# Optimization experiments

Measured on AMD Instinct MI355X. Metric: run time of the kernel, lower is better.

Reference implementation:

```python
import jax, jax.numpy as jnp
from jax import lax
import numpy as np

V, E, H, T, L = 100000, 300, 512, 11, 4096
START, STOP = 9, 10
NEG_INF = -10000.0


def setup_inputs() -> dict:
    key = jax.random.key(0)
    ks = jax.random.split(key, 14)
    n = lambda k, s, sc=0.1: jax.random.normal(k, s, dtype=jnp.float32) * sc
    transitions = jax.random.normal(ks[12], (T, T), dtype=jnp.float32)
    # __init__ pins transitions into START and out of STOP
    transitions = transitions.at[START, :].set(NEG_INF).at[:, STOP].set(NEG_INF)
    return {
        'sentence': jax.random.randint(ks[0], (L,), 0, V),
        'embedding': n(ks[1], (V, E), 1.0),
        'w_ih_f': n(ks[2], (4 * H, E)), 'w_hh_f': n(ks[3], (4 * H, H)),
        'b_ih_f': n(ks[4], (4 * H,)), 'b_hh_f': n(ks[5], (4 * H,)),
        'w_ih_b': n(ks[6], (4 * H, E)), 'w_hh_b': n(ks[7], (4 * H, H)),
        'b_ih_b': n(ks[8], (4 * H,)), 'b_hh_b': n(ks[9], (4 * H,)),
        'w_tag': n(ks[10], (T, 2 * H)), 'b_tag': n(ks[11], (T,)),
        'transitions': transitions,
    }


def _lstm(x, w_ih, w_hh, b_ih, b_hh, reverse):
    # x: [L, E]; PyTorch gate order i, f, g, o
    Hd = w_hh.shape[1]
    # precompute input projections for all timesteps: [L, 4H]
    xg = x @ w_ih.T + b_ih + b_hh
    def step(carry, xt):
        h, c = carry
        g = xt + w_hh @ h
        i, f, gg, o = jnp.split(g, 4)
        c = jax.nn.sigmoid(f) * c + jax.nn.sigmoid(i) * jnp.tanh(gg)
        h = jax.nn.sigmoid(o) * jnp.tanh(c)
        return (h, c), h
    init = (jnp.zeros((Hd,), x.dtype), jnp.zeros((Hd,), x.dtype))
    _, hs = lax.scan(step, init, xg, reverse=reverse)
    return hs  # [L, H]


def _get_lstm_features(sentence, embedding, w_ih_f, w_hh_f, b_ih_f, b_hh_f,
                       w_ih_b, w_hh_b, b_ih_b, b_hh_b, w_tag, b_tag):
    x = embedding[sentence]  # [L, E]
    hf = _lstm(x, w_ih_f, w_hh_f, b_ih_f, b_hh_f, reverse=False)
    hb = _lstm(x, w_ih_b, w_hh_b, b_ih_b, b_hh_b, reverse=True)
    h = jnp.concatenate([hf, hb], axis=-1)  # [L, 2H]
    return h @ w_tag.T + b_tag  # [L, T]


def _viterbi(feats, transitions):
    init = jnp.full((T,), NEG_INF, feats.dtype).at[START].set(0.0)
    def step(fv, feat):
        scores = fv[None, :] + transitions  # [T_next, T_prev]
        bptr = jnp.argmax(scores, axis=1)
        fv2 = jnp.max(scores, axis=1) + feat
        return fv2, bptr
    fv, bptrs = lax.scan(step, init, feats)  # bptrs: [L, T]
    terminal = fv + transitions[STOP]
    best = jnp.argmax(terminal)
    path_score = terminal[best]
    def back(tag, bp):
        return bp[tag], tag
    _, path = lax.scan(back, best, bptrs, reverse=True)  # tags for t=0..L-1
    return path_score, path


def reference(sentence, embedding, w_ih_f, w_hh_f, b_ih_f, b_hh_f,
              w_ih_b, w_hh_b, b_ih_b, b_hh_b, w_tag, b_tag, transitions):
    feats = _get_lstm_features(sentence, embedding, w_ih_f, w_hh_f, b_ih_f, b_hh_f,
                               w_ih_b, w_hh_b, b_ih_b, b_hh_b, w_tag, b_tag)
    return _viterbi(feats, transitions)
```

## Files before the change

kernel.cpp:

```cpp
#include <hip/hip_runtime.h>
#include <hip/hip_bf16.h>
#include <stdint.h>

#define LL 4096
#define EE 300
#define HH 512
#define G4H 2048
#define TT 11
#define TSTART 9
#define TSTOP 10
#define NEGINF -10000.0f

typedef unsigned long long u64;
typedef short short8 __attribute__((ext_vector_type(8)));
typedef float f32x4 __attribute__((ext_vector_type(4)));

__device__ __forceinline__ float sigf(float x){
    x = fminf(fmaxf(x, -30.f), 30.f);
    return 1.0f / (1.0f + __expf(-x));
}
__device__ __forceinline__ float tanhfast(float x){
    x = fminf(fmaxf(x, -15.f), 15.f);
    float e = __expf(-2.0f * x);
    return (1.0f - e) / (1.0f + e);
}
__device__ __forceinline__ u64 lda(const u64* p){
    return __hip_atomic_load(p, __ATOMIC_RELAXED, __HIP_MEMORY_SCOPE_AGENT);
}
__device__ __forceinline__ unsigned f2bf(float f){
    unsigned u = __float_as_uint(f);
    return ((u + 0x7FFFu + ((u >> 16) & 1u)) >> 16) & 0xFFFFu;
}

__global__ void k0_zero(u64* __restrict__ comm){
    int i = blockIdx.x * blockDim.x + threadIdx.x;
    if (i < 2 * 2 * HH) comm[i] = 0ull;
}

__global__ __launch_bounds__(256) void k1_xg(
    const int* __restrict__ sent, const float* __restrict__ emb,
    const float* __restrict__ wih_f, const float* __restrict__ bih_f, const float* __restrict__ bhh_f,
    const float* __restrict__ wih_b, const float* __restrict__ bih_b, const float* __restrict__ bhh_b,
    float* __restrict__ xg_f, float* __restrict__ xg_b)
{
    __shared__ float elds[32 * 304];
    int t0  = blockIdx.x * 32;
    int r0  = blockIdx.y * 256;
    int dir = blockIdx.z;
    const float* wih = dir ? wih_b : wih_f;
    const float* bih = dir ? bih_b : bih_f;
    const float* bhh = dir ? bhh_b : bhh_f;
    float* xg = dir ? xg_b : xg_f;

    for (int idx = threadIdx.x; idx < 32 * EE; idx += 256){
        int i = idx / EE, e = idx - i * EE;
        elds[i * 304 + e] = emb[(long)sent[t0 + i] * EE + e];
    }
    __syncthreads();

    int rA = r0 + (threadIdx.x & 127);
    int rB = rA + 128;
    int half = threadIdx.x >> 7;
    float accA[16], accB[16];
    #pragma unroll
    for (int i = 0; i < 16; i++){ accA[i] = 0.f; accB[i] = 0.f; }
    const float* wrowA = wih + (long)rA * EE;
    const float* wrowB = wih + (long)rB * EE;
    for (int e4 = 0; e4 < 75; e4++){
        float4 wa = *reinterpret_cast<const float4*>(wrowA + e4 * 4);
        float4 wb = *reinterpret_cast<const float4*>(wrowB + e4 * 4);
        #pragma unroll
        for (int i = 0; i < 16; i++){
            float4 ev = *reinterpret_cast<const float4*>(&elds[(half * 16 + i) * 304 + e4 * 4]);
            accA[i] += wa.x * ev.x + wa.y * ev.y + wa.z * ev.z + wa.w * ev.w;
            accB[i] += wb.x * ev.x + wb.y * ev.y + wb.z * ev.z + wb.w * ev.w;
        }
    }
    float bA = bih[rA] + bhh[rA];
    float bB = bih[rB] + bhh[rB];
    #pragma unroll
    for (int i = 0; i < 16; i++){
        int t = t0 + half * 16 + i;
        xg[(long)t * G4H + rA] = accA[i] + bA;
        xg[(long)t * G4H + rB] = accB[i] + bB;
    }
}

__global__ __launch_bounds__(256) void k2_lstm(
    const float* __restrict__ whh_f, const float* __restrict__ whh_b,
    const float* __restrict__ xg_f, const float* __restrict__ xg_b,
    float* __restrict__ hs_f, float* __restrict__ hs_b,
    u64* __restrict__ comm)
{
    int dir = blockIdx.x >> 5;
    int b   = blockIdx.x & 31;
    int j0  = b * 16;
    int tid = threadIdx.x;
    int v   = tid >> 6;
    int l   = tid & 63;
    int grp = l >> 4;
    int jmine = j0 + v * 4 + grp;

    const float* whh = dir ? whh_b : whh_f;
    const float* xg  = dir ? xg_b  : xg_f;
    float* hs        = dir ? hs_b  : hs_f;
    u64* cm          = comm + dir * 2 * HH;

    short8 afrag[16];
    {
        int m    = l & 15;
        int jloc = m >> 2;
        int g    = m & 3;
        const float* wp = whh + (size_t)(g * HH + j0 + v * 4 + jloc) * HH + (l >> 4) * 8;
        #pragma unroll
        for (int kc = 0; kc < 16; kc++){
            float4 w0 = *reinterpret_cast<const float4*>(wp + kc * 32);
            float4 w1 = *reinterpret_cast<const float4*>(wp + kc * 32 + 4);
            union { unsigned u[4]; short8 s; } fr;
            fr.u[0] = f2bf(w0.x) | (f2bf(w0.y) << 16);
            fr.u[1] = f2bf(w0.z) | (f2bf(w0.w) << 16);
            fr.u[2] = f2bf(w1.x) | (f2bf(w1.y) << 16);
            fr.u[3] = f2bf(w1.z) | (f2bf(w1.w) << 16);
            afrag[kc] = fr.s;
        }
    }

    __shared__ __align__(16) unsigned hb[2][256];
    float c = 0.f;

    for (int s = 0; s < LL; ++s){
        int t = dir ? (LL - 1 - s) : s;

        const float* xp = xg + (size_t)t * G4H + jmine;
        float xg0 = xp[0], xg1 = xp[HH], xg2 = xp[2 * HH], xg3 = xp[3 * HH];

        if (s > 0){
            u64* pw = cm + (s & 1) * HH + 2 * tid;
            u64 va = lda(pw), vb = lda(pw + 1);
            unsigned want = (unsigned)s;
            for (;;){
                bool ok = ((unsigned)(va >> 32) == want) && ((unsigned)(vb >> 32) == want);
                if (__all(ok)) break;
                if ((unsigned)(va >> 32) != want) va = lda(pw);
                if ((unsigned)(vb >> 32) != want) vb = lda(pw + 1);
            }
            hb[s & 1][tid] = f2bf(__uint_as_float((unsigned)va))
                           | (f2bf(__uint_as_float((unsigned)vb)) << 16);
        }
        __syncthreads();

        f32x4 acc = {0.f, 0.f, 0.f, 0.f};
        if (s > 0){
            const char* hbase = (const char*)&hb[s & 1][0] + grp * 16;
            #pragma unroll
            for (int kc = 0; kc < 16; kc++){
                short8 bfrag = *reinterpret_cast<const short8*>(hbase + kc * 64);
                acc = __builtin_amdgcn_mfma_f32_16x16x32_bf16(afrag[kc], bfrag, acc, 0, 0, 0);
            }
        }

        float vi = acc[0] + xg0;
        float vf = acc[1] + xg1;
        float vgg = acc[2] + xg2;
        float vo = acc[3] + xg3;
        c = sigf(vf) * c + sigf(vi) * tanhfast(vgg);
        float hv = sigf(vo) * tanhfast(c);

        if ((l & 15) == 0){
            union { float f; unsigned u; } cv; cv.f = hv;
            u64 pk = ((u64)(s + 1) << 32) | (u64)cv.u;
            __hip_atomic_store(cm + ((s + 1) & 1) * HH + jmine, pk,
                               __ATOMIC_RELAXED, __HIP_MEMORY_SCOPE_AGENT);
            hs[(size_t)t * HH + jmine] = hv;
        }
    }
}

__global__ __launch_bounds__(64) void k3_feats(
    const float* __restrict__ hs_f, const float* __restrict__ hs_b,
    const float* __restrict__ wtag, const float* __restrict__ btag,
    float* __restrict__ feats)
{
    int t = blockIdx.x;
    int lane = threadIdx.x;
    float hreg[16];
    #pragma unroll
    for (int q = 0; q < 16; q++){
        int k = q * 64 + lane;
        hreg[q] = (q < 8) ? hs_f[(long)t * HH + k] : hs_b[(long)t * HH + (k - HH)];
    }
    for (int n = 0; n < TT; n++){
        float a = 0.f;
        #pragma unroll
        for (int q = 0; q < 16; q++){
            a += wtag[n * 1024 + q * 64 + lane] * hreg[q];
        }
        #pragma unroll
        for (int off = 32; off; off >>= 1) a += __shfl_down(a, off, 64);
        if (lane == 0) feats[t * 12 + n] = a + btag[n];
    }
}

__global__ __launch_bounds__(64) void k4a_chunk(
    const float* __restrict__ feats, const float* __restrict__ trans,
    float* __restrict__ Pmat)
{
    int c = blockIdx.x;
    int lane = threadIdx.x;
    float tr[TT][TT];
    #pragma unroll
    for (int n = 0; n < TT; n++)
        #pragma unroll
        for (int p = 0; p < TT; p++) tr[n][p] = trans[n * TT + p];

    float pv[TT];
    #pragma unroll
    for (int n = 0; n < TT; n++) pv[n] = (n == lane) ? 0.f : NEGINF;

    for (int i = 0; i < 64; i++){
        int t = c * 64 + i;
        float ft[TT];
        #pragma unroll
        for (int n = 0; n < TT; n++) ft[n] = feats[t * 12 + n];
        float pn[TT];
        #pragma unroll
        for (int n = 0; n < TT; n++){
            float m = tr[n][0] + pv[0];
            #pragma unroll
            for (int p = 1; p < TT; p++) m = fmaxf(m, tr[n][p] + pv[p]);
            pn[n] = m + ft[n];
        }
        #pragma unroll
        for (int n = 0; n < TT; n++) pv[n] = pn[n];
    }
    if (lane < TT){
        #pragma unroll
        for (int n = 0; n < TT; n++) Pmat[(c * TT + n) * TT + lane] = pv[n];
    }
}

__global__ __launch_bounds__(64) void k4b_bound(
    const float* __restrict__ Pmat, float* __restrict__ fvb)
{
    int lane = threadIdx.x;
    int ln = (lane < TT) ? lane : 0;
    float fv[TT];
    #pragma unroll
    for (int n = 0; n < TT; n++) fv[n] = (n == TSTART) ? 0.f : NEGINF;

    for (int c = 0; c < 64; c++){
        if (lane < TT) fvb[c * TT + lane] = fv[lane];
        float nf = NEGINF;
        #pragma unroll
        for (int s = 0; s < TT; s++)
            nf = fmaxf(nf, Pmat[(c * TT + ln) * TT + s] + fv[s]);
        #pragma unroll
        for (int n = 0; n < TT; n++) fv[n] = __shfl(nf, n, 64);
    }
    if (lane < TT) fvb[64 * TT + lane] = fv[lane];
}

__global__ __launch_bounds__(64) void k4c_bp(
    const float* __restrict__ feats, const float* __restrict__ trans,
    const float* __restrict__ fvb, u64* __restrict__ bpw)
{
    int c = blockIdx.x;
    int lane = threadIdx.x;
    int ln = (lane < TT) ? lane : 0;
    float trl[TT];
    #pragma unroll
    for (int p = 0; p < TT; p++) trl[p] = trans[ln * TT + p];
    float fv[TT];
    #pragma unroll
    for (int n = 0; n < TT; n++) fv[n] = fvb[c * TT + n];

    for (int i = 0; i < 64; i++){
        int t = c * 64 + i;
        float best = NEGINF; int bp = 0;
        #pragma unroll
        for (int p = 0; p < TT; p++){
            float sp = trl[p] + fv[p];
            if (sp > best){ best = sp; bp = p; }
        }
        if (lane >= TT) bp = 0;
        unsigned lo = (lane < 8) ? ((unsigned)bp << (4 * lane)) : 0u;
        unsigned hi = (lane >= 8 && lane < TT) ? ((unsigned)bp << (4 * (lane - 8))) : 0u;
        #pragma unroll
        for (int off = 1; off < 16; off <<= 1){
            lo |= __shfl_xor(lo, off, 16); hi |= __shfl_xor(hi, off, 16);
        }
        if (lane == 0) bpw[t] = (u64)lo | ((u64)hi << 32);
        float nf = (lane < TT) ? best + feats[t * 12 + ln] : NEGINF;
        #pragma unroll
        for (int n = 0; n < TT; n++) fv[n] = __shfl(nf, n, 64);
    }
}

__global__ __launch_bounds__(256) void k4d_bt(
    const u64* __restrict__ bpw, const float* __restrict__ fvb,
    const float* __restrict__ trans, float* __restrict__ out)
{
    __shared__ u64 bl[LL];
    int tid = threadIdx.x;
    for (int i = tid; i < LL; i += 256) bl[i] = bpw[i];
    __syncthreads();

    if (tid < 64){
        int lane = tid;
        int ln = (lane < TT) ? lane : 0;
        float term = (lane < TT) ? (fvb[64 * TT + ln] + trans[TSTOP * TT + ln]) : -3.0e38f;
        int idx = (lane < TT) ? lane : 63;
        #pragma unroll
        for (int off = 32; off; off >>= 1){
            float os = __shfl_down(term, off, 64);
            int   oi = __shfl_down(idx,  off, 64);
            if (os > term || (os == term && oi < idx)){ term = os; idx = oi; }
        }
        if (lane == 0){
            out[0] = term;
            int tag = idx;
            out[1 + (LL - 1)] = (float)tag;
            for (int u = LL - 1; u >= 1; --u){
                tag = (int)((bl[u] >> (4 * tag)) & 15ull);
                out[u] = (float)tag;
            }
        }
    }
}

__global__ void k_dbg(float* out, float v){ out[0] = v; }

extern "C" void kernel_launch(void* const* d_in, const int* in_sizes, int n_in,
                              void* d_out, int out_size, void* d_ws, size_t ws_size,
                              hipStream_t stream)
{
    const int*   sent  = (const int*)  d_in[0];
    const float* emb   = (const float*)d_in[1];
    const float* wih_f = (const float*)d_in[2];
    const float* whh_f = (const float*)d_in[3];
    const float* bih_f = (const float*)d_in[4];
    const float* bhh_f = (const float*)d_in[5];
    const float* wih_b = (const float*)d_in[6];
    const float* whh_b = (const float*)d_in[7];
    const float* bih_b = (const float*)d_in[8];
    const float* bhh_b = (const float*)d_in[9];
    const float* wtag  = (const float*)d_in[10];
    const float* btag  = (const float*)d_in[11];
    const float* trans = (const float*)d_in[12];
    float* out = (float*)d_out;

    char* ws = (char*)d_ws;
    size_t off = 0;
    float* xg_f = (float*)(ws + off); off += (size_t)LL * G4H * 4;
    float* xg_b = (float*)(ws + off); off += (size_t)LL * G4H * 4;
    float* hs_f = (float*)(ws + off); off += (size_t)LL * HH * 4;
    float* hs_b = (float*)(ws + off); off += (size_t)LL * HH * 4;
    float* feats= (float*)(ws + off); off += (size_t)LL * 12 * 4;
    u64* comm   = (u64*)(ws + off);   off += 2 * 2 * HH * 8;
    float* Pmat = (float*)(ws + off); off += (size_t)64 * TT * TT * 4;
    float* fvb  = (float*)(ws + off); off += (size_t)65 * TT * 4 + 64;
    u64* bpw    = (u64*)(ws + off);   off += (size_t)LL * 8;

    if (off > ws_size){
        k_dbg<<<1, 1, 0, stream>>>(out, (float)ws_size);
        return;
    }

    k0_zero<<<8, 256, 0, stream>>>(comm);
    k1_xg<<<dim3(128, 8, 2), 256, 0, stream>>>(sent, emb, wih_f, bih_f, bhh_f,
                                               wih_b, bih_b, bhh_b, xg_f, xg_b);
    k2_lstm<<<64, 256, 0, stream>>>(whh_f, whh_b, xg_f, xg_b, hs_f, hs_b, comm);
    k3_feats<<<LL, 64, 0, stream>>>(hs_f, hs_b, wtag, btag, feats);
    k4a_chunk<<<64, 64, 0, stream>>>(feats, trans, Pmat);
    k4b_bound<<<1, 64, 0, stream>>>(Pmat, fvb);
    k4c_bp<<<64, 64, 0, stream>>>(feats, trans, fvb, bpw);
    k4d_bt<<<1, 256, 0, stream>>>(bpw, fvb, trans, out);
}
```

Measured before the change: 7.871 ms.

## Split LSTM block into dedicated poller and compute warps with split MFMA chains

The recurrent LSTM kernel now launches 512 threads per block. Four extra wavefronts only poll the cross-block hidden-state exchange and stage bf16 h into shared memory, while the original four wavefronts keep the weight fragments and do the MFMA and gate math. The polling loop pipelines two outstanding loads per slot, and the 16-deep dependent MFMA chain is split into four independent accumulators to shorten latency. The aim is to cut per-step serial latency, but the doubled barrier participation and a larger block risk extra synchronisation cost and register pressure.

```diff
diff --git a/kernel.cpp b/kernel.cpp
--- a/kernel.cpp
+++ b/kernel.cpp
@@ -86,7 +86,7 @@
     }
 }
 
-__global__ __launch_bounds__(256) void k2_lstm(
+__global__ __launch_bounds__(512) void k2_lstm(
     const float* __restrict__ whh_f, const float* __restrict__ whh_b,
     const float* __restrict__ xg_f, const float* __restrict__ xg_b,
     float* __restrict__ hs_f, float* __restrict__ hs_b,
@@ -96,82 +96,103 @@
     int b   = blockIdx.x & 31;
     int j0  = b * 16;
     int tid = threadIdx.x;
-    int v   = tid >> 6;
-    int l   = tid & 63;
-    int grp = l >> 4;
-    int jmine = j0 + v * 4 + grp;
 
     const float* whh = dir ? whh_b : whh_f;
     const float* xg  = dir ? xg_b  : xg_f;
     float* hs        = dir ? hs_b  : hs_f;
     u64* cm          = comm + dir * 2 * HH;
 
-    short8 afrag[16];
-    {
-        int m    = l & 15;
-        int jloc = m >> 2;
-        int g    = m & 3;
-        const float* wp = whh + (size_t)(g * HH + j0 + v * 4 + jloc) * HH + (l >> 4) * 8;
-        #pragma unroll
-        for (int kc = 0; kc < 16; kc++){
-            float4 w0 = *reinterpret_cast<const float4*>(wp + kc * 32);
-            float4 w1 = *reinterpret_cast<const float4*>(wp + kc * 32 + 4);
-            union { unsigned u[4]; short8 s; } fr;
-            fr.u[0] = f2bf(w0.x) | (f2bf(w0.y) << 16);
-            fr.u[1] = f2bf(w0.z) | (f2bf(w0.w) << 16);
-            fr.u[2] = f2bf(w1.x) | (f2bf(w1.y) << 16);
-            fr.u[3] = f2bf(w1.z) | (f2bf(w1.w) << 16);
-            afrag[kc] = fr.s;
-        }
-    }
-
     __shared__ __align__(16) unsigned hb[2][256];
-    float c = 0.f;
-
-    for (int s = 0; s < LL; ++s){
-        int t = dir ? (LL - 1 - s) : s;
-
-        const float* xp = xg + (size_t)t * G4H + jmine;
-        float xg0 = xp[0], xg1 = xp[HH], xg2 = xp[2 * HH], xg3 = xp[3 * HH];
-
-        if (s > 0){
-            u64* pw = cm + (s & 1) * HH + 2 * tid;
-            u64 va = lda(pw), vb = lda(pw + 1);
-            unsigned want = (unsigned)s;
-            for (;;){
-                bool ok = ((unsigned)(va >> 32) == want) && ((unsigned)(vb >> 32) == want);
-                if (__all(ok)) break;
-                if ((unsigned)(va >> 32) != want) va = lda(pw);
-                if ((unsigned)(vb >> 32) != want) vb = lda(pw + 1);
-            }
-            hb[s & 1][tid] = f2bf(__uint_as_float((unsigned)va))
-                           | (f2bf(__uint_as_float((unsigned)vb)) << 16);
-        }
-        __syncthreads();
-
-        f32x4 acc = {0.f, 0.f, 0.f, 0.f};
-        if (s > 0){
-            const char* hbase = (const char*)&hb[s & 1][0] + grp * 16;
+
+    if (tid >= 256){
+        int u = tid - 256;
+        for (int s = 0; s < LL; ++s){
+            if (s > 0){
+                u64* pw = cm + (s & 1) * HH + 2 * u;
+                unsigned want = (unsigned)s;
+                u64 a0 = lda(pw),     b0 = lda(pw + 1);
+                u64 a1 = lda(pw),     b1 = lda(pw + 1);
+                bool oka = false, okb = false;
+                unsigned ra = 0, rb = 0;
+                for (;;){
+                    if (!oka){
+                        if ((unsigned)(a0 >> 32) == want){ ra = (unsigned)a0; oka = true; }
+                        else { a0 = a1; a1 = lda(pw); }
+                    }
+                    if (!okb){
+                        if ((unsigned)(b0 >> 32) == want){ rb = (unsigned)b0; okb = true; }
+                        else { b0 = b1; b1 = lda(pw + 1); }
+                    }
+                    if (__all(oka && okb)) break;
+                }
+                hb[s & 1][u] = f2bf(__uint_as_float(ra))
+                             | (f2bf(__uint_as_float(rb)) << 16);
+            }
+            __syncthreads();
+        }
+    } else {
+        int v   = tid >> 6;
+        int l   = tid & 63;
+        int grp = l >> 4;
+        int jmine = j0 + v * 4 + grp;
+
+        short8 afrag[16];
+        {
+            int m    = l & 15;
+            int jloc = m >> 2;
+            int g    = m & 3;
+            const float* wp = whh + (size_t)(g * HH + j0 + v * 4 + jloc) * HH + (l >> 4) * 8;
             #pragma unroll
             for (int kc = 0; kc < 16; kc++){
-                short8 bfrag = *reinterpret_cast<const short8*>(hbase + kc * 64);
-                acc = __builtin_amdgcn_mfma_f32_16x16x32_bf16(afrag[kc], bfrag, acc, 0, 0, 0);
-            }
-        }
-
-        float vi = acc[0] + xg0;
-        float vf = acc[1] + xg1;
-        float vgg = acc[2] + xg2;
-        float vo = acc[3] + xg3;
-        c = sigf(vf) * c + sigf(vi) * tanhfast(vgg);
-        float hv = sigf(vo) * tanhfast(c);
-
-        if ((l & 15) == 0){
-            union { float f; unsigned u; } cv; cv.f = hv;
-            u64 pk = ((u64)(s + 1) << 32) | (u64)cv.u;
-            __hip_atomic_store(cm + ((s + 1) & 1) * HH + jmine, pk,
-                               __ATOMIC_RELAXED, __HIP_MEMORY_SCOPE_AGENT);
-            hs[(size_t)t * HH + jmine] = hv;
+                float4 w0 = *reinterpret_cast<const float4*>(wp + kc * 32);
+                float4 w1 = *reinterpret_cast<const float4*>(wp + kc * 32 + 4);
+                union { unsigned u[4]; short8 s; } fr;
+                fr.u[0] = f2bf(w0.x) | (f2bf(w0.y) << 16);
+                fr.u[1] = f2bf(w0.z) | (f2bf(w0.w) << 16);
+                fr.u[2] = f2bf(w1.x) | (f2bf(w1.y) << 16);
+                fr.u[3] = f2bf(w1.z) | (f2bf(w1.w) << 16);
+                afrag[kc] = fr.s;
+            }
+        }
+
+        float c = 0.f;
+        for (int s = 0; s < LL; ++s){
+            int t = dir ? (LL - 1 - s) : s;
+            const float* xp = xg + (size_t)t * G4H + jmine;
+            float xg0 = xp[0], xg1 = xp[HH], xg2 = xp[2 * HH], xg3 = xp[3 * HH];
+
+            __syncthreads();
+
+            f32x4 ac0 = {0.f,0.f,0.f,0.f}, ac1 = ac0, ac2 = ac0, ac3 = ac0;
+            if (s > 0){
+                const char* hbase = (const char*)&hb[s & 1][0] + grp * 16;
+                #pragma unroll
+                for (int kc = 0; kc < 4; kc++){
+                    short8 b0 = *reinterpret_cast<const short8*>(hbase + kc * 64);
+                    short8 b1 = *reinterpret_cast<const short8*>(hbase + (4 + kc) * 64);
+                    short8 b2 = *reinterpret_cast<const short8*>(hbase + (8 + kc) * 64);
+                    short8 b3 = *reinterpret_cast<const short8*>(hbase + (12 + kc) * 64);
+                    ac0 = __builtin_amdgcn_mfma_f32_16x16x32_bf16(afrag[kc],      b0, ac0, 0, 0, 0);
+                    ac1 = __builtin_amdgcn_mfma_f32_16x16x32_bf16(afrag[4 + kc],  b1, ac1, 0, 0, 0);
+                    ac2 = __builtin_amdgcn_mfma_f32_16x16x32_bf16(afrag[8 + kc],  b2, ac2, 0, 0, 0);
+                    ac3 = __builtin_amdgcn_mfma_f32_16x16x32_bf16(afrag[12 + kc], b3, ac3, 0, 0, 0);
+                }
+            }
+
+            float vi = ((ac0[0] + ac1[0]) + (ac2[0] + ac3[0])) + xg0;
+            float vf = ((ac0[1] + ac1[1]) + (ac2[1] + ac3[1])) + xg1;
+            float vgg= ((ac0[2] + ac1[2]) + (ac2[2] + ac3[2])) + xg2;
+            float vo = ((ac0[3] + ac1[3]) + (ac2[3] + ac3[3])) + xg3;
+            c = sigf(vf) * c + sigf(vi) * tanhfast(vgg);
+            float hv = sigf(vo) * tanhfast(c);
+
+            if ((l & 15) == 0){
+                union { float f; unsigned u; } cv; cv.f = hv;
+                u64 pk = ((u64)(s + 1) << 32) | (u64)cv.u;
+                __hip_atomic_store(cm + ((s + 1) & 1) * HH + jmine, pk,
+                                   __ATOMIC_RELAXED, __HIP_MEMORY_SCOPE_AGENT);
+                hs[(size_t)t * HH + jmine] = hv;
+            }
         }
     }
 }
@@ -369,7 +390,7 @@
     k0_zero<<<8, 256, 0, stream>>>(comm);
     k1_xg<<<dim3(128, 8, 2), 256, 0, stream>>>(sent, emb, wih_f, bih_f, bhh_f,
                                                wih_b, bih_b, bhh_b, xg_f, xg_b);
-    k2_lstm<<<64, 256, 0, stream>>>(whh_f, whh_b, xg_f, xg_b, hs_f, hs_b, comm);
+    k2_lstm<<<64, 512, 0, stream>>>(whh_f, whh_b, xg_f, xg_b, hs_f, hs_b, comm);
     k3_feats<<<LL, 64, 0, stream>>>(hs_f, hs_b, wtag, btag, feats);
     k4a_chunk<<<64, 64, 0, stream>>>(feats, trans, Pmat);
     k4b_bound<<<1, 64, 0, stream>>>(Pmat, fvb);
```

Result: slower. 10.79 ms (+37.1%).

## Replace MFMA recurrent matvec with fp16 dot2 across 8 waves plus LDS reduction

Applied to the files above, without the earlier changes.

The per-step recurrent matvec in the LSTM kernel now uses fp16 packed dot2 instructions instead of bf16 MFMA. Blocks grow to 512 threads, each wave covering a 64-element K slice of the 64 gate rows, and partial sums are reduced through shared memory. Each thread now polls a single flag word instead of two. Wave 0 then applies the gate nonlinearities and publishes h. The aim is to shorten the serial per-step latency, at the cost of an extra barrier per step and fp16 rather than bf16 rounding of weights and h.

```diff
diff --git a/kernel.cpp b/kernel.cpp
--- a/kernel.cpp
+++ b/kernel.cpp
@@ -1,5 +1,6 @@
 #include <hip/hip_runtime.h>
 #include <hip/hip_bf16.h>
+#include <hip/hip_fp16.h>
 #include <stdint.h>
 
 #define LL 4096
@@ -12,8 +13,7 @@
 #define NEGINF -10000.0f
 
 typedef unsigned long long u64;
-typedef short short8 __attribute__((ext_vector_type(8)));
-typedef float f32x4 __attribute__((ext_vector_type(4)));
+typedef _Float16 h2v __attribute__((ext_vector_type(2)));
 
 __device__ __forceinline__ float sigf(float x){
     x = fminf(fmaxf(x, -30.f), 30.f);
@@ -27,9 +27,12 @@
 __device__ __forceinline__ u64 lda(const u64* p){
     return __hip_atomic_load(p, __ATOMIC_RELAXED, __HIP_MEMORY_SCOPE_AGENT);
 }
-__device__ __forceinline__ unsigned f2bf(float f){
-    unsigned u = __float_as_uint(f);
-    return ((u + 0x7FFFu + ((u >> 16) & 1u)) >> 16) & 0xFFFFu;
+__device__ __forceinline__ h2v u2h(unsigned u){
+    union { unsigned v; h2v h; } c; c.v = u; return c.h;
+}
+__device__ __forceinline__ h2v pk(float a, float b){
+    auto r = __builtin_amdgcn_cvt_pkrtz(a, b);
+    union { decltype(r) x; h2v h; } c; c.x = r; return c.h;
 }
 
 __global__ void k0_zero(u64* __restrict__ comm){
@@ -86,7 +89,7 @@
     }
 }
 
-__global__ __launch_bounds__(256) void k2_lstm(
+__global__ __launch_bounds__(512) void k2_lstm(
     const float* __restrict__ whh_f, const float* __restrict__ whh_b,
     const float* __restrict__ xg_f, const float* __restrict__ xg_b,
     float* __restrict__ hs_f, float* __restrict__ hs_b,
@@ -96,82 +99,90 @@
     int b   = blockIdx.x & 31;
     int j0  = b * 16;
     int tid = threadIdx.x;
-    int v   = tid >> 6;
+    int w   = tid >> 6;
     int l   = tid & 63;
-    int grp = l >> 4;
-    int jmine = j0 + v * 4 + grp;
+    int g   = l >> 4;
+    int jl  = l & 15;
+    int row = g * HH + j0 + jl;
 
     const float* whh = dir ? whh_b : whh_f;
     const float* xg  = dir ? xg_b  : xg_f;
     float* hs        = dir ? hs_b  : hs_f;
     u64* cm          = comm + dir * 2 * HH;
 
-    short8 afrag[16];
+    h2v wreg[32];
     {
-        int m    = l & 15;
-        int jloc = m >> 2;
-        int g    = m & 3;
-        const float* wp = whh + (size_t)(g * HH + j0 + v * 4 + jloc) * HH + (l >> 4) * 8;
-        #pragma unroll
-        for (int kc = 0; kc < 16; kc++){
-            float4 w0 = *reinterpret_cast<const float4*>(wp + kc * 32);
-            float4 w1 = *reinterpret_cast<const float4*>(wp + kc * 32 + 4);
-            union { unsigned u[4]; short8 s; } fr;
-            fr.u[0] = f2bf(w0.x) | (f2bf(w0.y) << 16);
-            fr.u[1] = f2bf(w0.z) | (f2bf(w0.w) << 16);
-            fr.u[2] = f2bf(w1.x) | (f2bf(w1.y) << 16);
-            fr.u[3] = f2bf(w1.z) | (f2bf(w1.w) << 16);
-            afrag[kc] = fr.s;
-        }
-    }
-
-    __shared__ __align__(16) unsigned hb[2][256];
+        const float* wp = whh + (size_t)row * HH + w * 64;
+        #pragma unroll
+        for (int m = 0; m < 32; m += 2){
+            float4 v = *reinterpret_cast<const float4*>(wp + 2 * m);
+            wreg[m]     = pk(v.x, v.y);
+            wreg[m + 1] = pk(v.z, v.w);
+        }
+    }
+
+    __shared__ __align__(16) unsigned short hl16[2][HH];
+    __shared__ float plds[2][512];
     float c = 0.f;
 
     for (int s = 0; s < LL; ++s){
         int t = dir ? (LL - 1 - s) : s;
-
-        const float* xp = xg + (size_t)t * G4H + jmine;
-        float xg0 = xp[0], xg1 = xp[HH], xg2 = xp[2 * HH], xg3 = xp[3 * HH];
-
-        if (s > 0){
-            u64* pw = cm + (s & 1) * HH + 2 * tid;
-            u64 va = lda(pw), vb = lda(pw + 1);
+        float xgv = 0.f;
+        if (tid < 64) xgv = xg[(size_t)t * G4H + row];
+
+        if (s == 0){
+            hl16[0][tid] = 0;
+        } else {
+            const u64* pw = cm + (s & 1) * HH + tid;
+            u64 v = lda(pw);
             unsigned want = (unsigned)s;
-            for (;;){
-                bool ok = ((unsigned)(va >> 32) == want) && ((unsigned)(vb >> 32) == want);
-                if (__all(ok)) break;
-                if ((unsigned)(va >> 32) != want) va = lda(pw);
-                if ((unsigned)(vb >> 32) != want) vb = lda(pw + 1);
+            while (!__all((unsigned)(v >> 32) == want)){
+                if ((unsigned)(v >> 32) != want) v = lda(pw);
             }
-            hb[s & 1][tid] = f2bf(__uint_as_float((unsigned)va))
-                           | (f2bf(__uint_as_float((unsigned)vb)) << 16);
+            float hval = __uint_as_float((unsigned)v);
+            union { h2v h; unsigned u; } cv2; cv2.h = pk(hval, hval);
+            hl16[s & 1][tid] = (unsigned short)(cv2.u & 0xFFFFu);
         }
         __syncthreads();
 
-        f32x4 acc = {0.f, 0.f, 0.f, 0.f};
-        if (s > 0){
-            const char* hbase = (const char*)&hb[s & 1][0] + grp * 16;
+        float a0 = 0.f, a1 = 0.f, a2 = 0.f, a3 = 0.f;
+        {
+            const uint4* hseg = reinterpret_cast<const uint4*>(&hl16[s & 1][w * 64]);
             #pragma unroll
-            for (int kc = 0; kc < 16; kc++){
-                short8 bfrag = *reinterpret_cast<const short8*>(hbase + kc * 64);
-                acc = __builtin_amdgcn_mfma_f32_16x16x32_bf16(afrag[kc], bfrag, acc, 0, 0, 0);
+            for (int q = 0; q < 8; q += 2){
+                uint4 h0 = hseg[q];
+                uint4 h1 = hseg[q + 1];
+                a0 = __builtin_amdgcn_fdot2(wreg[4*q+0], u2h(h0.x), a0, false);
+                a1 = __builtin_amdgcn_fdot2(wreg[4*q+1], u2h(h0.y), a1, false);
+                a2 = __builtin_amdgcn_fdot2(wreg[4*q+2], u2h(h0.z), a2, false);
+                a3 = __builtin_amdgcn_fdot2(wreg[4*q+3], u2h(h0.w), a3, false);
+                a0 = __builtin_amdgcn_fdot2(wreg[4*q+4], u2h(h1.x), a0, false);
+                a1 = __builtin_amdgcn_fdot2(wreg[4*q+5], u2h(h1.y), a1, false);
+                a2 = __builtin_amdgcn_fdot2(wreg[4*q+6], u2h(h1.z), a2, false);
+                a3 = __builtin_amdgcn_fdot2(wreg[4*q+7], u2h(h1.w), a3, false);
             }
         }
-
-        float vi = acc[0] + xg0;
-        float vf = acc[1] + xg1;
-        float vgg = acc[2] + xg2;
-        float vo = acc[3] + xg3;
-        c = sigf(vf) * c + sigf(vi) * tanhfast(vgg);
-        float hv = sigf(vo) * tanhfast(c);
-
-        if ((l & 15) == 0){
-            union { float f; unsigned u; } cv; cv.f = hv;
-            u64 pk = ((u64)(s + 1) << 32) | (u64)cv.u;
-            __hip_atomic_store(cm + ((s + 1) & 1) * HH + jmine, pk,
-                               __ATOMIC_RELAXED, __HIP_MEMORY_SCOPE_AGENT);
-            hs[(size_t)t * HH + jmine] = hv;
+        plds[s & 1][tid] = (a0 + a1) + (a2 + a3);
+        __syncthreads();
+
+        if (w == 0){
+            float sum = 0.f;
+            #pragma unroll
+            for (int q = 0; q < 8; q++) sum += plds[s & 1][q * 64 + l];
+            float pre = sum + xgv;
+            float vi = __shfl(pre, jl,      64);
+            float vf = __shfl(pre, 16 + jl, 64);
+            float vg = __shfl(pre, 32 + jl, 64);
+            float vo = __shfl(pre, 48 + jl, 64);
+            c = sigf(vf) * c + sigf(vi) * tanhfast(vg);
+            float h = sigf(vo) * tanhfast(c);
+            if (l < 16){
+                union { float f; unsigned u; } hv; hv.f = h;
+                u64 pk2 = ((u64)(s + 1) << 32) | (u64)hv.u;
+                __hip_atomic_store(cm + ((s + 1) & 1) * HH + (j0 + l), pk2,
+                                   __ATOMIC_RELAXED, __HIP_MEMORY_SCOPE_AGENT);
+                hs[(size_t)t * HH + (j0 + l)] = h;
+            }
         }
     }
 }
@@ -369,7 +380,7 @@
     k0_zero<<<8, 256, 0, stream>>>(comm);
     k1_xg<<<dim3(128, 8, 2), 256, 0, stream>>>(sent, emb, wih_f, bih_f, bhh_f,
                                                wih_b, bih_b, bhh_b, xg_f, xg_b);
-    k2_lstm<<<64, 256, 0, stream>>>(whh_f, whh_b, xg_f, xg_b, hs_f, hs_b, comm);
+    k2_lstm<<<64, 512, 0, stream>>>(whh_f, whh_b, xg_f, xg_b, hs_f, hs_b, comm);
     k3_feats<<<LL, 64, 0, stream>>>(hs_f, hs_b, wtag, btag, feats);
     k4a_chunk<<<64, 64, 0, stream>>>(feats, trans, Pmat);
     k4b_bound<<<1, 64, 0, stream>>>(Pmat, fvb);
```

Result: faster. 6.633 ms (-15.7%).
